# Kernel tuning notes

Hardware: AMD Instinct MI355X
Metric: run time of the kernel (lower is better)

## Reference

```python
import jax, jax.numpy as jnp
import numpy as np

DIM = 1024
HEADS = 16
HEAD_DIM = DIM // HEADS
ROPE_BASE = 500000.0
SCALE = HEAD_DIM ** -0.5


def _rope_cos_sin(T, dtype=jnp.float32):
    inv_freq = 1.0 / (ROPE_BASE ** (jnp.arange(0, HEAD_DIM, 2, dtype=jnp.float32) / HEAD_DIM))
    t = jnp.arange(T, dtype=jnp.float32)
    freqs = t[:, None] * inv_freq[None, :]            # (T, hd/2)
    emb = jnp.concatenate([freqs, freqs], axis=-1)    # (T, hd)
    return jnp.cos(emb).astype(dtype), jnp.sin(emb).astype(dtype)


def _rotate_half(x):
    x1, x2 = jnp.split(x, 2, axis=-1)
    return jnp.concatenate([-x2, x1], axis=-1)


def _apply_rope(x, cos, sin):
    # x: (B,H,T,hd); cos/sin: (T,hd)
    return x * cos + _rotate_half(x) * sin


def setup_inputs() -> dict:
    key = jax.random.key(0)
    k1, k2, k3 = jax.random.split(key, 3)
    B, T = 4, 4096
    x = jax.random.normal(k1, (B, T, DIM), dtype=jnp.float32)
    W_qkv = jax.random.normal(k2, (DIM, 3 * DIM), dtype=jnp.float32) * (DIM ** -0.5)
    W_out = jax.random.normal(k3, (DIM, DIM), dtype=jnp.float32) * (DIM ** -0.5)
    return {"x": x, "W_qkv": W_qkv, "W_out": W_out}


def reference(x, W_qkv, W_out):
    B, T, D = x.shape
    H, hd = HEADS, HEAD_DIM
    qkv = (x @ W_qkv).reshape(B, T, 3, H, hd).transpose(2, 0, 3, 1, 4)  # (3,B,H,T,hd)
    q, k, v = qkv[0], qkv[1], qkv[2]
    cos, sin = _rope_cos_sin(T, q.dtype)
    q = _apply_rope(q, cos, sin)
    k = _apply_rope(k, cos, sin)
    # linear attention: elu+1 feature map
    q_feat = jax.nn.elu(q * SCALE) + 1.0
    k_feat = jax.nn.elu(k) + 1.0
    kv = jnp.einsum('bhtd,bhtv->bhdv', k_feat, v)      # (B,H,hd,hd)
    k_sum = k_feat.sum(axis=2)                          # (B,H,hd)
    denom = jnp.maximum(jnp.einsum('bhtd,bhd->bht', q_feat, k_sum), 1e-6)
    out = jnp.einsum('bhtd,bhdv->bhtv', q_feat, kv) / denom[..., None]
    out = out.transpose(0, 2, 1, 3).reshape(B, T, D)
    return out @ W_out
```

## Files before the change

kernel.cpp:

```cpp
#include <hip/hip_runtime.h>
#include <hip/hip_bf16.h>

typedef __bf16 bf16;
typedef bf16 bf16x4 __attribute__((ext_vector_type(4)));
typedef bf16 bf16x8 __attribute__((ext_vector_type(8)));
typedef float f32x4 __attribute__((ext_vector_type(4)));

#define GLD_LDS16(gptr, lptr) \
  __builtin_amdgcn_global_load_lds((const __attribute__((address_space(1))) unsigned int*)(gptr), \
                                   (__attribute__((address_space(3))) unsigned int*)(lptr), 16, 0, 0)

__global__ __launch_bounds__(256) void f32_to_bf16(const float* __restrict__ in,
                                                   bf16* __restrict__ out) {
  const size_t i = ((size_t)blockIdx.x * 256 + threadIdx.x) * 8;
  float4 a = *(const float4*)(in + i);
  float4 b = *(const float4*)(in + i + 4);
  bf16x8 o;
  o[0] = (bf16)a.x; o[1] = (bf16)a.y; o[2] = (bf16)a.z; o[3] = (bf16)a.w;
  o[4] = (bf16)b.x; o[5] = (bf16)b.y; o[6] = (bf16)b.z; o[7] = (bf16)b.w;
  *(bf16x8*)(out + i) = o;
}

__global__ __launch_bounds__(256) void transpose_f32_bf16(const float* __restrict__ in,
                                                          bf16* __restrict__ out,
                                                          int R, int C) {
  __shared__ float tile[32][33];
  const int bx = blockIdx.x * 32;
  const int by = blockIdx.y * 32;
  const int tx = threadIdx.x & 31;
  const int ty = threadIdx.x >> 5;
#pragma unroll
  for (int i = 0; i < 4; i++) {
    int r = by + ty + i * 8;
    tile[ty + i * 8][tx] = in[(size_t)r * C + bx + tx];
  }
  __syncthreads();
#pragma unroll
  for (int i = 0; i < 4; i++) {
    int r = bx + ty + i * 8;
    out[(size_t)r * R + by + tx] = (bf16)tile[tx][ty + i * 8];
  }
}

__global__ __launch_bounds__(256) void rope_tab(float2* __restrict__ ctab) {
  const int idx = blockIdx.x * 256 + threadIdx.x;
  const int t = idx >> 5, f = idx & 31;
  const float invf = (float)exp(-((double)f / 32.0) * log(500000.0));
  float sn, cs;
  sincosf((float)t * invf, &sn, &cs);
  ctab[idx] = make_float2(cs, sn);
}

__device__ __forceinline__ void gemm256_core(const bf16* __restrict__ A,
                                             const bf16* __restrict__ BT,
                                             const int K, const int m0, const int n0,
                                             bf16* __restrict__ As, bf16* __restrict__ Bs,
                                             f32x4 acc[8][4]) {
  const int tid = threadIdx.x;
  const int lane = tid & 63;
  const int w = tid >> 6;
  const int wm = w >> 2, wn = w & 3;

#pragma unroll
  for (int i = 0; i < 8; i++)
#pragma unroll
    for (int j = 0; j < 4; j++) acc[i][j] = f32x4{0.f, 0.f, 0.f, 0.f};

  const int rA = (w << 3) + (lane >> 3);
  const int colS = (((lane & 7) ^ ((lane >> 3) & 7)) << 3);
  const bf16* Ag = A + (size_t)(m0 + rA) * K + colS;
  const bf16* Bg = BT + (size_t)(n0 + rA) * K + colS;
  bf16* AsW = As + w * 512;
  bf16* BsW = Bs + w * 512;

#define STAGE2(G, L, h, k0)                                                        \
  do {                                                                             \
    GLD_LDS16((G) + (size_t)(h) * 128 * K + (k0), (L) + (h) * 8192);               \
    GLD_LDS16((G) + (size_t)(h) * 128 * K + (size_t)64 * K + (k0),                 \
              (L) + (h) * 8192 + 4096);                                            \
  } while (0)

  STAGE2(Ag, AsW, 0, 0);
  STAGE2(Ag, AsW, 1, 0);
  STAGE2(Bg, BsW, 0, 0);
  STAGE2(Bg, BsW, 1, 0);
  asm volatile("s_waitcnt vmcnt(0)" ::: "memory");
  __builtin_amdgcn_s_barrier();

  const int fr = lane & 15;
  const int kq = lane >> 4;
  const int swz = fr & 7;
  const int pc0 = ((kq) ^ swz) << 3;
  const int pc1 = ((4 + kq) ^ swz) << 3;

  bf16x8 af[4][2], bv[4][2];
  const int NT = K >> 6;

  for (int kt = 0; kt < NT; ++kt) {
    const int db = kt & 1;
    const bf16* Ah = As + db * 16384 + wm * 8192;
    const bf16* Bh = Bs + db * 16384 + (wn >> 1) * 8192;
    const int cb = (wn & 1) * 64;
    const int nk0 = (kt + 1) << 6;
    const bool stg = (kt + 1 < NT);
    bf16* AsN = AsW + (db ^ 1) * 16384;
    bf16* BsN = BsW + (db ^ 1) * 16384;

#pragma unroll
    for (int mi = 0; mi < 4; mi++) {
      af[mi][0] = *(const bf16x8*)(Ah + (mi * 16 + fr) * 64 + pc0);
      af[mi][1] = *(const bf16x8*)(Ah + (mi * 16 + fr) * 64 + pc1);
    }
#pragma unroll
    for (int ni = 0; ni < 2; ni++) {
      bv[ni][0] = *(const bf16x8*)(Bh + (cb + ni * 16 + fr) * 64 + pc0);
      bv[ni][1] = *(const bf16x8*)(Bh + (cb + ni * 16 + fr) * 64 + pc1);
    }
    if (stg) { STAGE2(Ag, AsN, 0, nk0); STAGE2(Ag, AsN, 1, nk0); }
    __builtin_amdgcn_s_barrier();
    asm volatile("s_waitcnt lgkmcnt(0)" ::: "memory");
    __builtin_amdgcn_sched_barrier(0);
    __builtin_amdgcn_s_setprio(1);
#pragma unroll
    for (int mi = 0; mi < 4; mi++)
#pragma unroll
      for (int ni = 0; ni < 2; ni++) {
        acc[mi][ni] = __builtin_amdgcn_mfma_f32_16x16x32_bf16(af[mi][0], bv[ni][0], acc[mi][ni], 0, 0, 0);
        acc[mi][ni] = __builtin_amdgcn_mfma_f32_16x16x32_bf16(af[mi][1], bv[ni][1], acc[mi][ni], 0, 0, 0);
      }
    __builtin_amdgcn_s_setprio(0);
    __builtin_amdgcn_s_barrier();

#pragma unroll
    for (int ni = 2; ni < 4; ni++) {
      bv[ni][0] = *(const bf16x8*)(Bh + (cb + ni * 16 + fr) * 64 + pc0);
      bv[ni][1] = *(const bf16x8*)(Bh + (cb + ni * 16 + fr) * 64 + pc1);
    }
    if (stg) STAGE2(Bg, BsN, 0, nk0);
    __builtin_amdgcn_s_barrier();
    asm volatile("s_waitcnt lgkmcnt(0)" ::: "memory");
    __builtin_amdgcn_sched_barrier(0);
    __builtin_amdgcn_s_setprio(1);
#pragma unroll
    for (int mi = 0; mi < 4; mi++)
#pragma unroll
      for (int ni = 2; ni < 4; ni++) {
        acc[mi][ni] = __builtin_amdgcn_mfma_f32_16x16x32_bf16(af[mi][0], bv[ni][0], acc[mi][ni], 0, 0, 0);
        acc[mi][ni] = __builtin_amdgcn_mfma_f32_16x16x32_bf16(af[mi][1], bv[ni][1], acc[mi][ni], 0, 0, 0);
      }
    __builtin_amdgcn_s_setprio(0);
    __builtin_amdgcn_s_barrier();

#pragma unroll
    for (int mi = 0; mi < 4; mi++) {
      af[mi][0] = *(const bf16x8*)(Ah + (64 + mi * 16 + fr) * 64 + pc0);
      af[mi][1] = *(const bf16x8*)(Ah + (64 + mi * 16 + fr) * 64 + pc1);
    }
    if (stg) STAGE2(Bg, BsN, 1, nk0);
    __builtin_amdgcn_s_barrier();
    asm volatile("s_waitcnt lgkmcnt(0)" ::: "memory");
    __builtin_amdgcn_sched_barrier(0);
    __builtin_amdgcn_s_setprio(1);
#pragma unroll
    for (int mi = 0; mi < 4; mi++)
#pragma unroll
      for (int ni = 2; ni < 4; ni++) {
        acc[mi + 4][ni] = __builtin_amdgcn_mfma_f32_16x16x32_bf16(af[mi][0], bv[ni][0], acc[mi + 4][ni], 0, 0, 0);
        acc[mi + 4][ni] = __builtin_amdgcn_mfma_f32_16x16x32_bf16(af[mi][1], bv[ni][1], acc[mi + 4][ni], 0, 0, 0);
      }
    __builtin_amdgcn_s_setprio(0);
    __builtin_amdgcn_s_barrier();

    __builtin_amdgcn_s_setprio(1);
#pragma unroll
    for (int mi = 0; mi < 4; mi++)
#pragma unroll
      for (int ni = 0; ni < 2; ni++) {
        acc[mi + 4][ni] = __builtin_amdgcn_mfma_f32_16x16x32_bf16(af[mi][0], bv[ni][0], acc[mi + 4][ni], 0, 0, 0);
        acc[mi + 4][ni] = __builtin_amdgcn_mfma_f32_16x16x32_bf16(af[mi][1], bv[ni][1], acc[mi + 4][ni], 0, 0, 0);
      }
    __builtin_amdgcn_s_setprio(0);
    asm volatile("s_waitcnt vmcnt(0)" ::: "memory");
    __builtin_amdgcn_s_barrier();
  }
#undef STAGE2
}

__device__ __forceinline__ void xcd_tile(int& m0, int& n0) {
  const int gx = gridDim.x;
  const int nwg = gx * gridDim.y;
  const int orig = blockIdx.y * gx + blockIdx.x;
  const int cpx = nwg >> 3;
  const int swb = (orig & 7) * cpx + (orig >> 3);
  m0 = (swb / gx) * 256;
  n0 = (swb % gx) * 256;
}

__global__ __launch_bounds__(512, 2) void gemm_qkv_fused(const bf16* __restrict__ A,
                                                         const bf16* __restrict__ BT,
                                                         const float2* __restrict__ ctab,
                                                         bf16* __restrict__ qfB,
                                                         bf16* __restrict__ kfB,
                                                         bf16* __restrict__ vfB) {
  __shared__ __attribute__((aligned(16))) bf16 As[32768];
  __shared__ __attribute__((aligned(16))) bf16 Bs[32768];
  const int K = 1024;
  int m0, n0;
  xcd_tile(m0, n0);

  f32x4 acc[8][4];
  gemm256_core(A, BT, K, m0, n0, As, Bs, acc);

  const int lane = threadIdx.x & 63;
  const int w = threadIdx.x >> 6;
  const int wm = w >> 2, wn = w & 3;
  const int fr15 = lane & 15;
  const int cb = n0 + wn * 64;
  const int p = cb >> 10;
  const int hh = (cb & 1023) >> 6;
  const int row00 = m0 + wm * 128 + ((lane >> 4) << 2);
  const int b = row00 >> 12;
  const size_t base0 = ((size_t)(b * 16 + hh)) * 4096 * 64;

  if (p == 2) {
#pragma unroll
    for (int mi = 0; mi < 8; mi++)
#pragma unroll
      for (int r = 0; r < 4; r++) {
        const int tloc = (row00 + mi * 16 + r) & 4095;
        bf16* dst = vfB + base0 + (size_t)tloc * 64;
#pragma unroll
        for (int ni = 0; ni < 4; ni++) dst[fr15 + ni * 16] = (bf16)acc[mi][ni][r];
      }
  } else {
    bf16* outp = (p == 0) ? qfB : kfB;
    const float scl = (p == 0) ? 0.125f : 1.0f;
#pragma unroll
    for (int mi = 0; mi < 8; mi++)
#pragma unroll
      for (int r = 0; r < 4; r++) {
        const int tloc = (row00 + mi * 16 + r) & 4095;
        const float2* ct = ctab + tloc * 32;
        bf16* dst = outp + base0 + (size_t)tloc * 64;
#pragma unroll
        for (int ni = 0; ni < 2; ni++) {
          const float2 cs2 = ct[fr15 + ni * 16];
          const float x1 = acc[mi][ni][r], x2 = acc[mi][ni + 2][r];
          const float r1 = (x1 * cs2.x - x2 * cs2.y) * scl;
          const float r2 = (x2 * cs2.x + x1 * cs2.y) * scl;
          dst[fr15 + ni * 16] = (bf16)(r1 > 0.f ? r1 + 1.f : __expf(r1));
          dst[fr15 + ni * 16 + 32] = (bf16)(r2 > 0.f ? r2 + 1.f : __expf(r2));
        }
      }
  }
}

__global__ __launch_bounds__(512, 2) void gemm_bt_f32(const bf16* __restrict__ A,
                                                      const bf16* __restrict__ BT,
                                                      float* __restrict__ C,
                                                      int N, int K) {
  __shared__ __attribute__((aligned(16))) bf16 As[32768];
  __shared__ __attribute__((aligned(16))) bf16 Bs[32768];
  int m0, n0;
  xcd_tile(m0, n0);

  f32x4 acc[8][4];
  gemm256_core(A, BT, K, m0, n0, As, Bs, acc);

  const int lane = threadIdx.x & 63;
  const int w = threadIdx.x >> 6;
  const int wm = w >> 2, wn = w & 3;
  const int col0 = n0 + wn * 64 + (lane & 15);
  const int row00 = m0 + wm * 128 + ((lane >> 4) << 2);
#pragma unroll
  for (int mi = 0; mi < 8; mi++)
#pragma unroll
    for (int ni = 0; ni < 4; ni++)
#pragma unroll
      for (int r = 0; r < 4; r++)
        C[(size_t)(row00 + mi * 16 + r) * N + col0 + ni * 16] = acc[mi][ni][r];
}

__global__ __launch_bounds__(256) void attn_kv(const bf16* __restrict__ kfB,
                                               const bf16* __restrict__ vfB,
                                               float* __restrict__ kvg,
                                               float* __restrict__ ksumg) {
  const int bh = blockIdx.x;
  const int t0 = blockIdx.y * 256;
  __shared__ __attribute__((aligned(16))) float kfs[32][68];
  __shared__ __attribute__((aligned(16))) float vfs[32][68];
  const int tid = threadIdx.x;
  const int dq = tid & 15, g = tid >> 4;
  const int tl = tid >> 3, ch = (tid & 7) * 8;

  f32x4 acc[4];
#pragma unroll
  for (int r = 0; r < 4; r++) acc[r] = f32x4{0.f, 0.f, 0.f, 0.f};
  float ksa[4] = {0.f, 0.f, 0.f, 0.f};

  for (int sc = 0; sc < 8; sc++) {
    const size_t rowb = ((size_t)bh * 4096 + t0 + sc * 32 + tl) * 64 + ch;
    bf16x8 k8 = *(const bf16x8*)(kfB + rowb);
    bf16x8 v8 = *(const bf16x8*)(vfB + rowb);
    f32x4 ka, kb, va, vb;
#pragma unroll
    for (int j = 0; j < 4; j++) {
      ka[j] = (float)k8[j]; kb[j] = (float)k8[j + 4];
      va[j] = (float)v8[j]; vb[j] = (float)v8[j + 4];
    }
    *(f32x4*)&kfs[tl][ch] = ka;
    *(f32x4*)&kfs[tl][ch + 4] = kb;
    *(f32x4*)&vfs[tl][ch] = va;
    *(f32x4*)&vfs[tl][ch + 4] = vb;
    __syncthreads();

#pragma unroll 8
    for (int t = 0; t < 32; t++) {
      f32x4 kq = *(const f32x4*)&kfs[t][dq * 4];
      f32x4 vq = *(const f32x4*)&vfs[t][g * 4];
#pragma unroll
      for (int r = 0; r < 4; r++) {
#pragma unroll
        for (int c = 0; c < 4; c++) acc[r][c] += kq[r] * vq[c];
      }
      if (g == 0) {
#pragma unroll
        for (int r = 0; r < 4; r++) ksa[r] += kq[r];
      }
    }
    __syncthreads();
  }

#pragma unroll
  for (int r = 0; r < 4; r++)
#pragma unroll
    for (int c = 0; c < 4; c++)
      atomicAdd(&kvg[(size_t)bh * 4096 + (dq * 4 + r) * 64 + g * 4 + c], acc[r][c]);
  if (g == 0) {
#pragma unroll
    for (int r = 0; r < 4; r++) atomicAdd(&ksumg[bh * 64 + dq * 4 + r], ksa[r]);
  }
}

__global__ __launch_bounds__(256) void attn_out(const bf16* __restrict__ qfB,
                                                const float* __restrict__ kvg,
                                                const float* __restrict__ ksumg,
                                                bf16* __restrict__ attn) {
  const int bh = blockIdx.y;
  const int b = bh >> 4, h = bh & 15;
  const int t0 = blockIdx.x * 64;
  __shared__ __attribute__((aligned(16))) float qf[64][68];
  __shared__ __attribute__((aligned(16))) float kvs[64][64];
  __shared__ __attribute__((aligned(16))) float ksums[64];
  const int tid = threadIdx.x;

#pragma unroll
  for (int j = 0; j < 2; j++) {
    int chunk = tid + 256 * j;
    int tl = chunk >> 3, col = (chunk & 7) * 8;
    bf16x8 r = *(const bf16x8*)(qfB + ((size_t)bh * 4096 + t0 + tl) * 64 + col);
    f32x4 a, bb;
#pragma unroll
    for (int q = 0; q < 4; q++) { a[q] = (float)r[q]; bb[q] = (float)r[q + 4]; }
    *(f32x4*)&qf[tl][col] = a;
    *(f32x4*)&qf[tl][col + 4] = bb;
  }
#pragma unroll
  for (int j = 0; j < 4; j++) {
    int idx = tid + 256 * j;
    *(float4*)&kvs[idx >> 4][(idx & 15) * 4] = *(const float4*)&kvg[(size_t)bh * 4096 + idx * 4];
  }
  if (tid < 64) ksums[tid] = ksumg[bh * 64 + tid];
  __syncthreads();

  const int tr = tid >> 4, cc = tid & 15;
  f32x4 acc[4];
#pragma unroll
  for (int r = 0; r < 4; r++) acc[r] = f32x4{0.f, 0.f, 0.f, 0.f};
  f32x4 dn = f32x4{0.f, 0.f, 0.f, 0.f};

  for (int d2 = 0; d2 < 64; d2++) {
    f32x4 kv4 = *(const f32x4*)&kvs[d2][cc * 4];
    float ks = ksums[d2];
#pragma unroll
    for (int r = 0; r < 4; r++) {
      float qv = qf[tr * 4 + r][d2];
      acc[r] += qv * kv4;
      dn[r] += qv * ks;
    }
  }

#pragma unroll
  for (int r = 0; r < 4; r++) {
    const float rdn = 1.f / fmaxf(dn[r], 1e-6f);
    bf16x4 o;
#pragma unroll
    for (int c = 0; c < 4; c++) o[c] = (bf16)(acc[r][c] * rdn);
    *(bf16x4*)(attn + ((size_t)(b * 4096) + t0 + tr * 4 + r) * 1024 + h * 64 + cc * 4) = o;
  }
}

extern "C" void kernel_launch(void* const* d_in, const int* in_sizes, int n_in,
                              void* d_out, int out_size, void* d_ws, size_t ws_size,
                              hipStream_t stream) {
  if (ws_size < 177225728ULL) return;

  const float* x = (const float*)d_in[0];
  const float* Wqkv = (const float*)d_in[1];
  const float* Wout = (const float*)d_in[2];
  float* out = (float*)d_out;
  char* ws = (char*)d_ws;

  float* kvg = (float*)(ws);
  float* ksumg = (float*)(ws + 1048576);
  bf16* WqkvT = (bf16*)(ws + 1064960);
  bf16* WoutT = (bf16*)(ws + 7356416);
  bf16* attn = (bf16*)(ws + 9453568);
  float2* ctab = (float2*)(ws + 9453568);
  bf16* qfB = (bf16*)(ws + 43008000);
  bf16* kfB = (bf16*)(ws + 76562432);
  bf16* vfB = (bf16*)(ws + 110116864);
  bf16* xB = (bf16*)(ws + 143671296);

  hipMemsetAsync(ws, 0, 1048576 + 16384, stream);

  rope_tab<<<512, 256, 0, stream>>>(ctab);
  f32_to_bf16<<<16777216 / (256 * 8), 256, 0, stream>>>(x, xB);
  transpose_f32_bf16<<<dim3(3072 / 32, 1024 / 32), 256, 0, stream>>>(Wqkv, WqkvT, 1024, 3072);
  transpose_f32_bf16<<<dim3(1024 / 32, 1024 / 32), 256, 0, stream>>>(Wout, WoutT, 1024, 1024);

  gemm_qkv_fused<<<dim3(3072 / 256, 16384 / 256), 512, 0, stream>>>(xB, WqkvT, ctab, qfB, kfB, vfB);

  attn_kv<<<dim3(64, 16), 256, 0, stream>>>(kfB, vfB, kvg, ksumg);
  attn_out<<<dim3(64, 64), 256, 0, stream>>>(qfB, kvg, ksumg, attn);

  gemm_bt_f32<<<dim3(1024 / 256, 16384 / 256), 512, 0, stream>>>(attn, WoutT, out, 1024, 1024);
}
```

Measured before the change: 385.9 us.

## Split K tile into half-stages with deeper global-to-LDS prefetch pipeline

Restructures the 256x256 GEMM core so each 64-wide K tile is staged as two 32-wide halves in separate LDS buffers, with a new swizzle and fragment layout. Loads for the next half-stage are issued up to two halves ahead, and the wait uses partial vmcnt counts instead of draining all loads every iteration. Each half now does 32 MFMAs with 8 A and 4 B fragments, replacing four smaller phases with many barriers. This is meant to overlap memory with compute better and reduce barrier count, at the cost of more register pressure and fragile vmcnt accounting.

New measurement: 385.3 us. No clear change (-0.2%).

```diff
diff --git a/kernel.cpp b/kernel.cpp
--- a/kernel.cpp
+++ b/kernel.cpp
@@ -66,124 +66,84 @@
 #pragma unroll
     for (int j = 0; j < 4; j++) acc[i][j] = f32x4{0.f, 0.f, 0.f, 0.f};
 
-  const int rA = (w << 3) + (lane >> 3);
-  const int colS = (((lane & 7) ^ ((lane >> 3) & 7)) << 3);
-  const bf16* Ag = A + (size_t)(m0 + rA) * K + colS;
-  const bf16* Bg = BT + (size_t)(n0 + rA) * K + colS;
-  bf16* AsW = As + w * 512;
-  bf16* BsW = Bs + w * 512;
-
-#define STAGE2(G, L, h, k0)                                                        \
-  do {                                                                             \
-    GLD_LDS16((G) + (size_t)(h) * 128 * K + (k0), (L) + (h) * 8192);               \
-    GLD_LDS16((G) + (size_t)(h) * 128 * K + (size_t)64 * K + (k0),                 \
-              (L) + (h) * 8192 + 4096);                                            \
+  const int lch = (tid & 3) ^ ((tid >> 3) & 3);
+  const bf16* Ag = A + (size_t)(m0 + (tid >> 2)) * K + lch * 8;
+  const bf16* Bg = BT + (size_t)(n0 + (tid >> 2)) * K + lch * 8;
+  const int wb = w * 512;
+
+#define STG(kh, db, k0)                                                   \
+  do {                                                                    \
+    bf16* aD = As + ((db) * 2 + (kh)) * 8192 + wb;                        \
+    bf16* bD = Bs + ((db) * 2 + (kh)) * 8192 + wb;                        \
+    const size_t go = (size_t)(k0) + (kh) * 32;                           \
+    GLD_LDS16(Ag + go, aD);                                               \
+    GLD_LDS16(Ag + (size_t)128 * K + go, aD + 4096);                      \
+    GLD_LDS16(Bg + go, bD);                                               \
+    GLD_LDS16(Bg + (size_t)128 * K + go, bD + 4096);                      \
   } while (0)
-
-  STAGE2(Ag, AsW, 0, 0);
-  STAGE2(Ag, AsW, 1, 0);
-  STAGE2(Bg, BsW, 0, 0);
-  STAGE2(Bg, BsW, 1, 0);
-  asm volatile("s_waitcnt vmcnt(0)" ::: "memory");
-  __builtin_amdgcn_s_barrier();
 
   const int fr = lane & 15;
   const int kq = lane >> 4;
-  const int swz = fr & 7;
-  const int pc0 = ((kq) ^ swz) << 3;
-  const int pc1 = ((4 + kq) ^ swz) << 3;
-
-  bf16x8 af[4][2], bv[4][2];
+  const int frow = fr * 32 + ((kq ^ ((fr >> 1) & 3)) << 3);
+  const int aro = wm * 4096;
+  const int bro = wn * 2048;
+
+#define LOADFRAGS(kh, db)                                                 \
+  const bf16* Ap = As + ((db) * 2 + (kh)) * 8192 + aro + frow;            \
+  const bf16* Bp = Bs + ((db) * 2 + (kh)) * 8192 + bro + frow;            \
+  bf16x8 af[8], bv[4];                                                    \
+  _Pragma("unroll") for (int mi = 0; mi < 8; mi++)                        \
+      af[mi] = *(const bf16x8*)(Ap + mi * 512);                           \
+  _Pragma("unroll") for (int ni = 0; ni < 4; ni++)                        \
+      bv[ni] = *(const bf16x8*)(Bp + ni * 512);
+
+#define MFMA32                                                            \
+  __builtin_amdgcn_s_setprio(1);                                          \
+  _Pragma("unroll") for (int mi = 0; mi < 8; mi++)                        \
+  _Pragma("unroll") for (int ni = 0; ni < 4; ni++)                        \
+      acc[mi][ni] = __builtin_amdgcn_mfma_f32_16x16x32_bf16(              \
+          af[mi], bv[ni], acc[mi][ni], 0, 0, 0);                          \
+  __builtin_amdgcn_s_setprio(0);
+
+  STG(0, 0, 0);
+  STG(1, 0, 0);
+  if (K > 64) {
+    STG(0, 1, 64);
+    asm volatile("s_waitcnt vmcnt(8)" ::: "memory");
+  } else {
+    asm volatile("s_waitcnt vmcnt(4)" ::: "memory");
+  }
+  __builtin_amdgcn_s_barrier();
+
   const int NT = K >> 6;
-
   for (int kt = 0; kt < NT; ++kt) {
     const int db = kt & 1;
-    const bf16* Ah = As + db * 16384 + wm * 8192;
-    const bf16* Bh = Bs + db * 16384 + (wn >> 1) * 8192;
-    const int cb = (wn & 1) * 64;
-    const int nk0 = (kt + 1) << 6;
-    const bool stg = (kt + 1 < NT);
-    bf16* AsN = AsW + (db ^ 1) * 16384;
-    bf16* BsN = BsW + (db ^ 1) * 16384;
-
-#pragma unroll
-    for (int mi = 0; mi < 4; mi++) {
-      af[mi][0] = *(const bf16x8*)(Ah + (mi * 16 + fr) * 64 + pc0);
-      af[mi][1] = *(const bf16x8*)(Ah + (mi * 16 + fr) * 64 + pc1);
-    }
-#pragma unroll
-    for (int ni = 0; ni < 2; ni++) {
-      bv[ni][0] = *(const bf16x8*)(Bh + (cb + ni * 16 + fr) * 64 + pc0);
-      bv[ni][1] = *(const bf16x8*)(Bh + (cb + ni * 16 + fr) * 64 + pc1);
-    }
-    if (stg) { STAGE2(Ag, AsN, 0, nk0); STAGE2(Ag, AsN, 1, nk0); }
-    __builtin_amdgcn_s_barrier();
-    asm volatile("s_waitcnt lgkmcnt(0)" ::: "memory");
-    __builtin_amdgcn_sched_barrier(0);
-    __builtin_amdgcn_s_setprio(1);
-#pragma unroll
-    for (int mi = 0; mi < 4; mi++)
-#pragma unroll
-      for (int ni = 0; ni < 2; ni++) {
-        acc[mi][ni] = __builtin_amdgcn_mfma_f32_16x16x32_bf16(af[mi][0], bv[ni][0], acc[mi][ni], 0, 0, 0);
-        acc[mi][ni] = __builtin_amdgcn_mfma_f32_16x16x32_bf16(af[mi][1], bv[ni][1], acc[mi][ni], 0, 0, 0);
-      }
-    __builtin_amdgcn_s_setprio(0);
-    __builtin_amdgcn_s_barrier();
-
-#pragma unroll
-    for (int ni = 2; ni < 4; ni++) {
-      bv[ni][0] = *(const bf16x8*)(Bh + (cb + ni * 16 + fr) * 64 + pc0);
-      bv[ni][1] = *(const bf16x8*)(Bh + (cb + ni * 16 + fr) * 64 + pc1);
-    }
-    if (stg) STAGE2(Bg, BsN, 0, nk0);
-    __builtin_amdgcn_s_barrier();
-    asm volatile("s_waitcnt lgkmcnt(0)" ::: "memory");
-    __builtin_amdgcn_sched_barrier(0);
-    __builtin_amdgcn_s_setprio(1);
-#pragma unroll
-    for (int mi = 0; mi < 4; mi++)
-#pragma unroll
-      for (int ni = 2; ni < 4; ni++) {
-        acc[mi][ni] = __builtin_amdgcn_mfma_f32_16x16x32_bf16(af[mi][0], bv[ni][0], acc[mi][ni], 0, 0, 0);
-        acc[mi][ni] = __builtin_amdgcn_mfma_f32_16x16x32_bf16(af[mi][1], bv[ni][1], acc[mi][ni], 0, 0, 0);
-      }
-    __builtin_amdgcn_s_setprio(0);
-    __builtin_amdgcn_s_barrier();
-
-#pragma unroll
-    for (int mi = 0; mi < 4; mi++) {
-      af[mi][0] = *(const bf16x8*)(Ah + (64 + mi * 16 + fr) * 64 + pc0);
-      af[mi][1] = *(const bf16x8*)(Ah + (64 + mi * 16 + fr) * 64 + pc1);
-    }
-    if (stg) STAGE2(Bg, BsN, 1, nk0);
-    __builtin_amdgcn_s_barrier();
-    asm volatile("s_waitcnt lgkmcnt(0)" ::: "memory");
-    __builtin_amdgcn_sched_barrier(0);
-    __builtin_amdgcn_s_setprio(1);
-#pragma unroll
-    for (int mi = 0; mi < 4; mi++)
-#pragma unroll
-      for (int ni = 2; ni < 4; ni++) {
-        acc[mi + 4][ni] = __builtin_amdgcn_mfma_f32_16x16x32_bf16(af[mi][0], bv[ni][0], acc[mi + 4][ni], 0, 0, 0);
-        acc[mi + 4][ni] = __builtin_amdgcn_mfma_f32_16x16x32_bf16(af[mi][1], bv[ni][1], acc[mi + 4][ni], 0, 0, 0);
-      }
-    __builtin_amdgcn_s_setprio(0);
-    __builtin_amdgcn_s_barrier();
-
-    __builtin_amdgcn_s_setprio(1);
-#pragma unroll
-    for (int mi = 0; mi < 4; mi++)
-#pragma unroll
-      for (int ni = 0; ni < 2; ni++) {
-        acc[mi + 4][ni] = __builtin_amdgcn_mfma_f32_16x16x32_bf16(af[mi][0], bv[ni][0], acc[mi + 4][ni], 0, 0, 0);
-        acc[mi + 4][ni] = __builtin_amdgcn_mfma_f32_16x16x32_bf16(af[mi][1], bv[ni][1], acc[mi + 4][ni], 0, 0, 0);
-      }
-    __builtin_amdgcn_s_setprio(0);
-    asm volatile("s_waitcnt vmcnt(0)" ::: "memory");
-    __builtin_amdgcn_s_barrier();
-  }
-#undef STAGE2
+    {
+      LOADFRAGS(0, db);
+      if (kt + 1 < NT) STG(1, db ^ 1, (kt + 1) * 64);
+      __builtin_amdgcn_s_barrier();
+      asm volatile("s_waitcnt lgkmcnt(0)" ::: "memory");
+      __builtin_amdgcn_sched_barrier(0);
+      MFMA32;
+      if (kt + 1 < NT) asm volatile("s_waitcnt vmcnt(8)" ::: "memory");
+      else             asm volatile("s_waitcnt vmcnt(0)" ::: "memory");
+      __builtin_amdgcn_s_barrier();
+    }
+    {
+      LOADFRAGS(1, db);
+      if (kt + 2 < NT) STG(0, db, (kt + 2) * 64);
+      __builtin_amdgcn_s_barrier();
+      asm volatile("s_waitcnt lgkmcnt(0)" ::: "memory");
+      __builtin_amdgcn_sched_barrier(0);
+      MFMA32;
+      if (kt + 2 < NT)      asm volatile("s_waitcnt vmcnt(8)" ::: "memory");
+      else if (kt + 1 < NT) asm volatile("s_waitcnt vmcnt(4)" ::: "memory");
+      __builtin_amdgcn_s_barrier();
+    }
+  }
+#undef STG
+#undef LOADFRAGS
+#undef MFMA32
 }
 
 __device__ __forceinline__ void xcd_tile(int& m0, int& n0) {
```
